# Kernel tuning notes

Hardware: AMD Instinct MI355X
Metric: run time of the kernel (lower is better)

Reference implementation:

```python
import jax, jax.numpy as jnp
import numpy as np

B, T, U, D, NCLS = 4, 256, 128, 512, 1024


def setup_inputs() -> dict:
    key = jax.random.key(0)
    k1, k2, k3, k4, k5, k6 = jax.random.split(key, 6)
    s = 1.0 / np.sqrt(2 * D)  # ~ torch Linear init scale for fan_in=2D
    s2 = 1.0 / np.sqrt(D)
    return {
        "encoder_outputs": jax.random.normal(k1, (B, T, D), jnp.float32),
        "decoder_outputs": jax.random.normal(k2, (B, U, D), jnp.float32),
        "W_e": jax.random.normal(k3, (D, D), jnp.float32) * s,
        "W_d": jax.random.normal(k4, (D, D), jnp.float32) * s,
        "b1": jax.random.normal(k5, (D,), jnp.float32) * s,
        "W2": jax.random.normal(k6, (D, NCLS), jnp.float32) * s2,
    }


def reference(encoder_outputs, decoder_outputs, W_e, W_d, b1, W2):
    # RNNT joint. Original: broadcast-repeat enc to (B,T,U,D) and dec to
    # (B,T,U,D), concat along last dim, Linear(2D->D), tanh, Linear(D->NCLS,
    # no bias), log_softmax. Splitting the first Linear's weight into the
    # encoder half W_e and decoder half W_d gives identical math without
    # materializing the (B,T,U,2D) concat.
    enc_proj = jnp.einsum('btd,dh->bth', encoder_outputs, W_e)  # (B,T,D)
    dec_proj = jnp.einsum('bud,dh->buh', decoder_outputs, W_d)  # (B,U,D)
    hidden = jnp.tanh(enc_proj[:, :, None, :] + dec_proj[:, None, :, :] + b1)  # (B,T,U,D)
    logits = jnp.einsum('btuh,hc->btuc', hidden, W2)  # (B,T,U,NCLS)
    return jax.nn.log_softmax(logits, axis=-1)
```

## Files before the change

### kernel.cpp

```cpp
#include <hip/hip_runtime.h>


#define BB 4
#define TT 256
#define UU 128
#define DD 512
#define CC 1024

using f32x16 = __attribute__((ext_vector_type(16))) float;
using bf16x8 = __attribute__((ext_vector_type(8))) __bf16;

static __device__ __forceinline__ unsigned short f2bf(float f) {
    unsigned int u = __float_as_uint(f);
    unsigned int r = (u + 0x7FFFu + ((u >> 16) & 1u)) >> 16;
    return (unsigned short)r;
}

static __device__ __forceinline__ float tanh_fast(float x) {
    float a = x * 2.8853900817779268f;
    a = fminf(30.f, fmaxf(-30.f, a));
    float e = __expf(a * 0.6931471805599453f);
    float r = __builtin_amdgcn_rcpf(e + 1.0f);
    return __builtin_fmaf(-2.f, r, 1.f);
}

__global__ __launch_bounds__(256) void proj_fused(
    const float* __restrict__ enc, const float* __restrict__ dec,
    const float* __restrict__ W_e, const float* __restrict__ W_d,
    const float* __restrict__ b1,
    float* __restrict__ ep, float* __restrict__ dp)
{
    __shared__ float As[32][34];
    __shared__ float Ws[32][68];
    const int mb = blockIdx.x * 32;
    const int n0 = blockIdx.y * 64;
    const bool is_enc = (mb < BB * TT);
    const float* A = is_enc ? enc + (size_t)mb * DD
                            : dec + (size_t)(mb - BB * TT) * DD;
    const float* W = is_enc ? W_e : W_d;
    float* C = is_enc ? ep + (size_t)mb * DD
                      : dp + (size_t)(mb - BB * TT) * DD;
    const int tid = threadIdx.x;
    const int tx = tid & 15, ty = tid >> 4;
    float acc[2][4] = {};
    for (int k0 = 0; k0 < DD; k0 += 32) {
        __syncthreads();
        {
            const int row = tid >> 3, kk = (tid & 7) * 4;
            float4 v = *reinterpret_cast<const float4*>(A + (size_t)row * DD + k0 + kk);
            As[kk][row] = v.x; As[kk + 1][row] = v.y;
            As[kk + 2][row] = v.z; As[kk + 3][row] = v.w;
            const int wk = tid >> 3, wc2 = (tid & 7) * 8;
            float4 w0 = *reinterpret_cast<const float4*>(W + (size_t)(k0 + wk) * DD + n0 + wc2);
            float4 w1 = *reinterpret_cast<const float4*>(W + (size_t)(k0 + wk) * DD + n0 + wc2 + 4);
            *reinterpret_cast<float4*>(&Ws[wk][wc2]) = w0;
            *reinterpret_cast<float4*>(&Ws[wk][wc2 + 4]) = w1;
        }
        __syncthreads();
        #pragma unroll 4
        for (int kk = 0; kk < 32; ++kk) {
            float a0 = As[kk][ty * 2], a1 = As[kk][ty * 2 + 1];
            float w0 = Ws[kk][tx * 4], w1 = Ws[kk][tx * 4 + 1];
            float w2 = Ws[kk][tx * 4 + 2], w3 = Ws[kk][tx * 4 + 3];
            acc[0][0] += a0 * w0; acc[0][1] += a0 * w1;
            acc[0][2] += a0 * w2; acc[0][3] += a0 * w3;
            acc[1][0] += a1 * w0; acc[1][1] += a1 * w1;
            acc[1][2] += a1 * w2; acc[1][3] += a1 * w3;
        }
    }
    float bb[4] = {0.f, 0.f, 0.f, 0.f};
    if (is_enc) {
        #pragma unroll
        for (int j = 0; j < 4; ++j) bb[j] = b1[n0 + tx * 4 + j];
    }
    #pragma unroll
    for (int i = 0; i < 2; ++i) {
        float4 v;
        v.x = acc[i][0] + bb[0]; v.y = acc[i][1] + bb[1];
        v.z = acc[i][2] + bb[2]; v.w = acc[i][3] + bb[3];
        *reinterpret_cast<float4*>(C + (size_t)(ty * 2 + i) * DD + n0 + tx * 4) = v;
    }
}

__global__ __launch_bounds__(256) void pack_w2(
    const float* __restrict__ W2, unsigned short* __restrict__ w2p)
{
    int i = blockIdx.x * 256 + threadIdx.x;
    int k = i >> 10, c = i & 1023;
    int idx = (((k >> 3) * CC) + c) * 8 + (k & 7);
    w2p[idx] = f2bf(W2[i]);
}

__global__ __launch_bounds__(1024, 4) void joint_kernel(
    const float* __restrict__ ep, const float* __restrict__ dp,
    const unsigned short* __restrict__ w2p, float* __restrict__ out)
{
    __shared__ __align__(16) unsigned char ldsA[64 * 1024];
    __shared__ float maxw[64][9];
    __shared__ float sumw[64][9];

    const int bid = blockIdx.x;
    const int bt  = bid >> 1;
    const int u0  = (bid & 1) * 64;
    const int b   = bt >> 8;
    const int tid = threadIdx.x;

    {
        const int row = tid >> 4;
        const int kq  = tid & 15;
        const float* eprow = ep + (size_t)bt * DD;
        const float* dprow = dp + (size_t)(b * UU + u0 + row) * DD;
        #pragma unroll
        for (int c = 0; c < 4; ++c) {
            const int ktag = kq + c * 16;
            const int k0 = ktag * 8;
            float4 e0 = *reinterpret_cast<const float4*>(eprow + k0);
            float4 e1 = *reinterpret_cast<const float4*>(eprow + k0 + 4);
            float4 d0 = *reinterpret_cast<const float4*>(dprow + k0);
            float4 d1 = *reinterpret_cast<const float4*>(dprow + k0 + 4);
            float h0 = tanh_fast(e0.x + d0.x), h1 = tanh_fast(e0.y + d0.y);
            float h2 = tanh_fast(e0.z + d0.z), h3 = tanh_fast(e0.w + d0.w);
            float h4 = tanh_fast(e1.x + d1.x), h5 = tanh_fast(e1.y + d1.y);
            float h6 = tanh_fast(e1.z + d1.z), h7 = tanh_fast(e1.w + d1.w);
            uint4 pk;
            pk.x = (unsigned)f2bf(h0) | ((unsigned)f2bf(h1) << 16);
            pk.y = (unsigned)f2bf(h2) | ((unsigned)f2bf(h3) << 16);
            pk.z = (unsigned)f2bf(h4) | ((unsigned)f2bf(h5) << 16);
            pk.w = (unsigned)f2bf(h6) | ((unsigned)f2bf(h7) << 16);
            const int rsw = ((row ^ ktag) & 31) | (row & 32);
            *reinterpret_cast<uint4*>(ldsA + ktag * 1024 + rsw * 16) = pk;
        }
    }
    __syncthreads();

    const int lane = tid & 63;
    const int w    = tid >> 6;
    const int g    = lane >> 5;
    const int l31  = lane & 31;
    const int ur   = w >> 3;
    const int wc   = w & 7;

    const unsigned char* hidbase = ldsA + ur * 512;
    const unsigned short* wpbase = w2p + (size_t)(g * 1024 + wc * 128 + l31) * 8;

    f32x16 acc0 = {}, acc1 = {}, acc2 = {}, acc3 = {};

    #define LDH(kk) (*reinterpret_cast<const bf16x8*>(hidbase \
        + ((((kk) & 31) * 2 + g) * 1024) \
        + ((l31 ^ (((((kk) & 31) * 2 + g)) & 31)) << 4)))
    #define LDW(kk, t) (*reinterpret_cast<const bf16x8*>(wpbase \
        + ((size_t)((kk) & 31) * 16384) + (t) * 256))

    bf16x8 wv0 = LDW(0, 0), wv1 = LDW(0, 1), wv2 = LDW(0, 2), wv3 = LDW(0, 3);

    #pragma unroll 2
    for (int kk = 0; kk < 32; ++kk) {
        bf16x8 hf = LDH(kk);
        bf16x8 n0 = LDW(kk + 1, 0), n1 = LDW(kk + 1, 1);
        bf16x8 n2 = LDW(kk + 1, 2), n3 = LDW(kk + 1, 3);
        acc0 = __builtin_amdgcn_mfma_f32_32x32x16_bf16(wv0, hf, acc0, 0, 0, 0);
        acc1 = __builtin_amdgcn_mfma_f32_32x32x16_bf16(wv1, hf, acc1, 0, 0, 0);
        acc2 = __builtin_amdgcn_mfma_f32_32x32x16_bf16(wv2, hf, acc2, 0, 0, 0);
        acc3 = __builtin_amdgcn_mfma_f32_32x32x16_bf16(wv3, hf, acc3, 0, 0, 0);
        wv0 = n0; wv1 = n1; wv2 = n2; wv3 = n3;
    }
    #undef LDH
    #undef LDW

    const int row = ur * 32 + l31;
    float rmloc = -3.0e38f;
    #pragma unroll
    for (int r = 0; r < 16; ++r)
        rmloc = fmaxf(rmloc, fmaxf(fmaxf(acc0[r], acc1[r]), fmaxf(acc2[r], acc3[r])));
    rmloc = fmaxf(rmloc, __shfl_xor(rmloc, 32, 64));
    if (lane < 32) maxw[row][wc] = rmloc;
    __syncthreads();
    float rmax = maxw[row][0];
    #pragma unroll
    for (int j = 1; j < 8; ++j) rmax = fmaxf(rmax, maxw[row][j]);
    float s = 0.f;
    #pragma unroll
    for (int r = 0; r < 16; ++r)
        s += __expf(acc0[r] - rmax) + __expf(acc1[r] - rmax)
           + __expf(acc2[r] - rmax) + __expf(acc3[r] - rmax);
    s += __shfl_xor(s, 32, 64);
    if (lane < 32) sumw[row][wc] = s;
    __syncthreads();
    float tot = 0.f;
    #pragma unroll
    for (int j = 0; j < 8; ++j) tot += sumw[row][j];
    const float lse = rmax + __logf(tot);
    const float lse_r = __shfl(lse, lane >> 1, 64);

    unsigned char* slot = ldsA + w * 4096;
    const int rr = lane >> 1, seg = lane & 1;
    float* outbase = out + ((size_t)(bt * UU + u0 + ur * 32)) * CC + wc * 128;

    #define CHUNK(T, ACC) { \
        _Pragma("unroll") \
        for (int j = 0; j < 4; ++j) { \
            float4 v; \
            v.x = ACC[4 * j]; v.y = ACC[4 * j + 1]; \
            v.z = ACC[4 * j + 2]; v.w = ACC[4 * j + 3]; \
            const int cg = 2 * j + g; \
            *reinterpret_cast<float4*>(slot + l31 * 128 + ((cg ^ (l31 & 7)) << 4)) = v; \
        } \
        asm volatile("s_waitcnt lgkmcnt(0)" ::: "memory"); \
        float4 q0 = *reinterpret_cast<const float4*>(slot + rr * 128 + (((seg * 4 + 0) ^ (rr & 7)) << 4)); \
        float4 q1 = *reinterpret_cast<const float4*>(slot + rr * 128 + (((seg * 4 + 1) ^ (rr & 7)) << 4)); \
        float4 q2 = *reinterpret_cast<const float4*>(slot + rr * 128 + (((seg * 4 + 2) ^ (rr & 7)) << 4)); \
        float4 q3 = *reinterpret_cast<const float4*>(slot + rr * 128 + (((seg * 4 + 3) ^ (rr & 7)) << 4)); \
        float* op = outbase + (size_t)rr * CC + (T) * 32 + seg * 16; \
        q0.x -= lse_r; q0.y -= lse_r; q0.z -= lse_r; q0.w -= lse_r; \
        q1.x -= lse_r; q1.y -= lse_r; q1.z -= lse_r; q1.w -= lse_r; \
        q2.x -= lse_r; q2.y -= lse_r; q2.z -= lse_r; q2.w -= lse_r; \
        q3.x -= lse_r; q3.y -= lse_r; q3.z -= lse_r; q3.w -= lse_r; \
        *reinterpret_cast<float4*>(op + 0)  = q0; \
        *reinterpret_cast<float4*>(op + 4)  = q1; \
        *reinterpret_cast<float4*>(op + 8)  = q2; \
        *reinterpret_cast<float4*>(op + 12) = q3; \
        asm volatile("s_waitcnt lgkmcnt(0)" ::: "memory"); \
    }
    CHUNK(0, acc0)
    CHUNK(1, acc1)
    CHUNK(2, acc2)
    CHUNK(3, acc3)
    #undef CHUNK
}

extern "C" void kernel_launch(void* const* d_in, const int* in_sizes, int n_in,
                              void* d_out, int out_size, void* d_ws, size_t ws_size,
                              hipStream_t stream) {
    const float* enc = (const float*)d_in[0];
    const float* dec = (const float*)d_in[1];
    const float* W_e = (const float*)d_in[2];
    const float* W_d = (const float*)d_in[3];
    const float* b1  = (const float*)d_in[4];
    const float* W2  = (const float*)d_in[5];
    float* out = (float*)d_out;

    char* ws = (char*)d_ws;
    float* ep = (float*)(ws);
    float* dp = (float*)(ws + (2u << 20));
    unsigned short* w2p = (unsigned short*)(ws + (3u << 20));

    hipLaunchKernelGGL(pack_w2, dim3((DD * CC) / 256), dim3(256), 0, stream, W2, w2p);
    hipLaunchKernelGGL(proj_fused, dim3((BB * TT + BB * UU) / 32, DD / 64), dim3(256), 0,
                       stream, enc, dec, W_e, W_d, b1, ep, dp);
    hipLaunchKernelGGL(joint_kernel, dim3(BB * TT * 2), dim3(1024), 0, stream,
                       ep, dp, w2p, out);
}
```

Before: 400.0 us.

## Stage W2 tiles into LDS with double-buffered async loads and retile waves

The joint kernel now streams each 32 KB k-slice of packed W2 into LDS with global_load_lds, double-buffered so the next slice loads during the current MFMAs. Each wave then covers a 64x64 output tile with a 2x2 set of MFMA accumulators, instead of a 32x128 tile fed by per-wave global loads of W2. The intent is to replace redundant per-wave L2 reads of W2 with one shared LDS copy. The output stores also become nontemporal to keep the large log-softmax output from polluting cache. In exchange it adds a block-wide barrier every k step, with only four MFMAs per wave between barriers, and roughly doubles LDS use, which can lower occupancy.

```diff
diff --git a/kernel.cpp b/kernel.cpp
--- a/kernel.cpp
+++ b/kernel.cpp
@@ -8,6 +8,7 @@
 #define CC 1024
 
 using f32x16 = __attribute__((ext_vector_type(16))) float;
+using f32x4  = __attribute__((ext_vector_type(4))) float;
 using bf16x8 = __attribute__((ext_vector_type(8))) __bf16;
 
 static __device__ __forceinline__ unsigned short f2bf(float f) {
@@ -22,6 +23,12 @@
     float e = __expf(a * 0.6931471805599453f);
     float r = __builtin_amdgcn_rcpf(e + 1.0f);
     return __builtin_fmaf(-2.f, r, 1.f);
+}
+
+static __device__ __forceinline__ void gl2lds16(const void* g, void* l) {
+    __builtin_amdgcn_global_load_lds(
+        (const __attribute__((address_space(1))) void*)g,
+        (__attribute__((address_space(3))) void*)l, 16, 0, 0);
 }
 
 __global__ __launch_bounds__(256) void proj_fused(
@@ -91,19 +98,23 @@
     w2p[idx] = f2bf(W2[i]);
 }
 
-__global__ __launch_bounds__(1024, 4) void joint_kernel(
+__global__ __launch_bounds__(1024, 4) void joint_lds(
     const float* __restrict__ ep, const float* __restrict__ dp,
     const unsigned short* __restrict__ w2p, float* __restrict__ out)
 {
-    __shared__ __align__(16) unsigned char ldsA[64 * 1024];
-    __shared__ float maxw[64][9];
-    __shared__ float sumw[64][9];
-
-    const int bid = blockIdx.x;
-    const int bt  = bid >> 1;
-    const int u0  = (bid & 1) * 64;
+    __shared__ __align__(16) unsigned char hidL[64 * 1024];
+    __shared__ __align__(16) unsigned char wbA[32768];
+    __shared__ __align__(16) unsigned char wbB[32768];
+    __shared__ float maxb[64][17];
+    __shared__ float sumb[64][17];
+
+    const int r   = blockIdx.x;
+    const int bt  = r >> 1;
+    const int u0  = (r & 1) * 64;
     const int b   = bt >> 8;
     const int tid = threadIdx.x;
+
+    const unsigned char* w2g = (const unsigned char*)w2p;
 
     {
         const int row = tid >> 4;
@@ -128,8 +139,10 @@
             pk.z = (unsigned)f2bf(h4) | ((unsigned)f2bf(h5) << 16);
             pk.w = (unsigned)f2bf(h6) | ((unsigned)f2bf(h7) << 16);
             const int rsw = ((row ^ ktag) & 31) | (row & 32);
-            *reinterpret_cast<uint4*>(ldsA + ktag * 1024 + rsw * 16) = pk;
-        }
+            *reinterpret_cast<uint4*>(hidL + ktag * 1024 + rsw * 16) = pk;
+        }
+        gl2lds16(w2g + tid * 16,         wbA + tid * 16);
+        gl2lds16(w2g + 16384 + tid * 16, wbA + 16384 + tid * 16);
     }
     __syncthreads();
 
@@ -137,94 +150,97 @@
     const int w    = tid >> 6;
     const int g    = lane >> 5;
     const int l31  = lane & 31;
-    const int ur   = w >> 3;
-    const int wc   = w & 7;
-
-    const unsigned char* hidbase = ldsA + ur * 512;
-    const unsigned short* wpbase = w2p + (size_t)(g * 1024 + wc * 128 + l31) * 8;
-
-    f32x16 acc0 = {}, acc1 = {}, acc2 = {}, acc3 = {};
-
-    #define LDH(kk) (*reinterpret_cast<const bf16x8*>(hidbase \
-        + ((((kk) & 31) * 2 + g) * 1024) \
-        + ((l31 ^ (((((kk) & 31) * 2 + g)) & 31)) << 4)))
-    #define LDW(kk, t) (*reinterpret_cast<const bf16x8*>(wpbase \
-        + ((size_t)((kk) & 31) * 16384) + (t) * 256))
-
-    bf16x8 wv0 = LDW(0, 0), wv1 = LDW(0, 1), wv2 = LDW(0, 2), wv3 = LDW(0, 3);
-
-    #pragma unroll 2
-    for (int kk = 0; kk < 32; ++kk) {
-        bf16x8 hf = LDH(kk);
-        bf16x8 n0 = LDW(kk + 1, 0), n1 = LDW(kk + 1, 1);
-        bf16x8 n2 = LDW(kk + 1, 2), n3 = LDW(kk + 1, 3);
-        acc0 = __builtin_amdgcn_mfma_f32_32x32x16_bf16(wv0, hf, acc0, 0, 0, 0);
-        acc1 = __builtin_amdgcn_mfma_f32_32x32x16_bf16(wv1, hf, acc1, 0, 0, 0);
-        acc2 = __builtin_amdgcn_mfma_f32_32x32x16_bf16(wv2, hf, acc2, 0, 0, 0);
-        acc3 = __builtin_amdgcn_mfma_f32_32x32x16_bf16(wv3, hf, acc3, 0, 0, 0);
-        wv0 = n0; wv1 = n1; wv2 = n2; wv3 = n3;
-    }
-    #undef LDH
-    #undef LDW
-
-    const int row = ur * 32 + l31;
-    float rmloc = -3.0e38f;
-    #pragma unroll
-    for (int r = 0; r < 16; ++r)
-        rmloc = fmaxf(rmloc, fmaxf(fmaxf(acc0[r], acc1[r]), fmaxf(acc2[r], acc3[r])));
-    rmloc = fmaxf(rmloc, __shfl_xor(rmloc, 32, 64));
-    if (lane < 32) maxw[row][wc] = rmloc;
+
+    unsigned char* curb = wbA;
+    unsigned char* nxtb = wbB;
+
+    f32x16 acc00 = {}, acc01 = {}, acc10 = {}, acc11 = {};
+
+    #define MFMA __builtin_amdgcn_mfma_f32_32x32x16_bf16
+    for (int kb = 0; kb < 32; ++kb) {
+        if (kb < 31) {
+            const unsigned char* src = w2g + (size_t)(kb + 1) * 32768;
+            gl2lds16(src + tid * 16,         nxtb + tid * 16);
+            gl2lds16(src + 16384 + tid * 16, nxtb + 16384 + tid * 16);
+        }
+        const int ktag = 2 * kb + g;
+        const int rs = ((l31 ^ ktag) & 31) << 4;
+        bf16x8 h0 = *reinterpret_cast<const bf16x8*>(hidL + ktag * 1024 + rs);
+        bf16x8 h1 = *reinterpret_cast<const bf16x8*>(hidL + ktag * 1024 + 512 + rs);
+        bf16x8 a0 = *reinterpret_cast<const bf16x8*>(curb + ((g * 1024 + w * 64 + l31) << 4));
+        bf16x8 a1 = *reinterpret_cast<const bf16x8*>(curb + ((g * 1024 + w * 64 + 32 + l31) << 4));
+        acc00 = MFMA(a0, h0, acc00, 0, 0, 0);
+        acc01 = MFMA(a0, h1, acc01, 0, 0, 0);
+        acc10 = MFMA(a1, h0, acc10, 0, 0, 0);
+        acc11 = MFMA(a1, h1, acc11, 0, 0, 0);
+        __syncthreads();
+        unsigned char* t = curb; curb = nxtb; nxtb = t;
+    }
+    #undef MFMA
+
+    float m0 = -3.0e38f, m1 = -3.0e38f;
+    #pragma unroll
+    for (int q = 0; q < 16; ++q) {
+        m0 = fmaxf(m0, fmaxf(acc00[q], acc10[q]));
+        m1 = fmaxf(m1, fmaxf(acc01[q], acc11[q]));
+    }
+    m0 = fmaxf(m0, __shfl_xor(m0, 32, 64));
+    m1 = fmaxf(m1, __shfl_xor(m1, 32, 64));
+    if (lane < 32) { maxb[l31][w] = m0; maxb[32 + l31][w] = m1; }
     __syncthreads();
-    float rmax = maxw[row][0];
-    #pragma unroll
-    for (int j = 1; j < 8; ++j) rmax = fmaxf(rmax, maxw[row][j]);
-    float s = 0.f;
-    #pragma unroll
-    for (int r = 0; r < 16; ++r)
-        s += __expf(acc0[r] - rmax) + __expf(acc1[r] - rmax)
-           + __expf(acc2[r] - rmax) + __expf(acc3[r] - rmax);
-    s += __shfl_xor(s, 32, 64);
-    if (lane < 32) sumw[row][wc] = s;
+    float rmax0 = maxb[l31][0], rmax1 = maxb[32 + l31][0];
+    #pragma unroll
+    for (int j = 1; j < 16; ++j) {
+        rmax0 = fmaxf(rmax0, maxb[l31][j]);
+        rmax1 = fmaxf(rmax1, maxb[32 + l31][j]);
+    }
+    float s0 = 0.f, s1 = 0.f;
+    #pragma unroll
+    for (int q = 0; q < 16; ++q) {
+        s0 += __expf(acc00[q] - rmax0) + __expf(acc10[q] - rmax0);
+        s1 += __expf(acc01[q] - rmax1) + __expf(acc11[q] - rmax1);
+    }
+    s0 += __shfl_xor(s0, 32, 64);
+    s1 += __shfl_xor(s1, 32, 64);
+    if (lane < 32) { sumb[l31][w] = s0; sumb[32 + l31][w] = s1; }
     __syncthreads();
-    float tot = 0.f;
-    #pragma unroll
-    for (int j = 0; j < 8; ++j) tot += sumw[row][j];
-    const float lse = rmax + __logf(tot);
-    const float lse_r = __shfl(lse, lane >> 1, 64);
-
-    unsigned char* slot = ldsA + w * 4096;
+    float t0 = 0.f, t1 = 0.f;
+    #pragma unroll
+    for (int j = 0; j < 16; ++j) { t0 += sumb[l31][j]; t1 += sumb[32 + l31][j]; }
+    const float lse0 = rmax0 + __logf(t0);
+    const float lse1 = rmax1 + __logf(t1);
+
+    unsigned char* slot = hidL + w * 4096;
     const int rr = lane >> 1, seg = lane & 1;
-    float* outbase = out + ((size_t)(bt * UU + u0 + ur * 32)) * CC + wc * 128;
-
-    #define CHUNK(T, ACC) { \
+    const float lse_r0 = __shfl(lse0, rr, 64);
+    const float lse_r1 = __shfl(lse1, rr, 64);
+    float* outbase = out + (size_t)r * 64 * CC + w * 64;
+
+    #define CHUNK(MR, T, ACC, LSER) { \
         _Pragma("unroll") \
         for (int j = 0; j < 4; ++j) { \
-            float4 v; \
+            f32x4 v; \
             v.x = ACC[4 * j]; v.y = ACC[4 * j + 1]; \
             v.z = ACC[4 * j + 2]; v.w = ACC[4 * j + 3]; \
-            const int cg = 2 * j + g; \
-            *reinterpret_cast<float4*>(slot + l31 * 128 + ((cg ^ (l31 & 7)) << 4)) = v; \
+            *reinterpret_cast<f32x4*>(slot + l31 * 128 + (((2 * j + g) ^ (l31 & 7)) << 4)) = v; \
         } \
         asm volatile("s_waitcnt lgkmcnt(0)" ::: "memory"); \
-        float4 q0 = *reinterpret_cast<const float4*>(slot + rr * 128 + (((seg * 4 + 0) ^ (rr & 7)) << 4)); \
-        float4 q1 = *reinterpret_cast<const float4*>(slot + rr * 128 + (((seg * 4 + 1) ^ (rr & 7)) << 4)); \
-        float4 q2 = *reinterpret_cast<const float4*>(slot + rr * 128 + (((seg * 4 + 2) ^ (rr & 7)) << 4)); \
-        float4 q3 = *reinterpret_cast<const float4*>(slot + rr * 128 + (((seg * 4 + 3) ^ (rr & 7)) << 4)); \
-        float* op = outbase + (size_t)rr * CC + (T) * 32 + seg * 16; \
-        q0.x -= lse_r; q0.y -= lse_r; q0.z -= lse_r; q0.w -= lse_r; \
-        q1.x -= lse_r; q1.y -= lse_r; q1.z -= lse_r; q1.w -= lse_r; \
-        q2.x -= lse_r; q2.y -= lse_r; q2.z -= lse_r; q2.w -= lse_r; \
-        q3.x -= lse_r; q3.y -= lse_r; q3.z -= lse_r; q3.w -= lse_r; \
-        *reinterpret_cast<float4*>(op + 0)  = q0; \
-        *reinterpret_cast<float4*>(op + 4)  = q1; \
-        *reinterpret_cast<float4*>(op + 8)  = q2; \
-        *reinterpret_cast<float4*>(op + 12) = q3; \
+        f32x4 q0 = *reinterpret_cast<const f32x4*>(slot + rr * 128 + (((seg * 4 + 0) ^ (rr & 7)) << 4)); \
+        f32x4 q1 = *reinterpret_cast<const f32x4*>(slot + rr * 128 + (((seg * 4 + 1) ^ (rr & 7)) << 4)); \
+        f32x4 q2 = *reinterpret_cast<const f32x4*>(slot + rr * 128 + (((seg * 4 + 2) ^ (rr & 7)) << 4)); \
+        f32x4 q3 = *reinterpret_cast<const f32x4*>(slot + rr * 128 + (((seg * 4 + 3) ^ (rr & 7)) << 4)); \
+        float* op = outbase + (size_t)((MR) * 32 + rr) * CC + (T) * 32 + seg * 16; \
+        q0 -= LSER; q1 -= LSER; q2 -= LSER; q3 -= LSER; \
+        __builtin_nontemporal_store(q0, reinterpret_cast<f32x4*>(op + 0)); \
+        __builtin_nontemporal_store(q1, reinterpret_cast<f32x4*>(op + 4)); \
+        __builtin_nontemporal_store(q2, reinterpret_cast<f32x4*>(op + 8)); \
+        __builtin_nontemporal_store(q3, reinterpret_cast<f32x4*>(op + 12)); \
         asm volatile("s_waitcnt lgkmcnt(0)" ::: "memory"); \
     }
-    CHUNK(0, acc0)
-    CHUNK(1, acc1)
-    CHUNK(2, acc2)
-    CHUNK(3, acc3)
+    CHUNK(0, 0, acc00, lse_r0)
+    CHUNK(0, 1, acc10, lse_r0)
+    CHUNK(1, 0, acc01, lse_r1)
+    CHUNK(1, 1, acc11, lse_r1)
     #undef CHUNK
 }
 
@@ -247,6 +263,6 @@
     hipLaunchKernelGGL(pack_w2, dim3((DD * CC) / 256), dim3(256), 0, stream, W2, w2p);
     hipLaunchKernelGGL(proj_fused, dim3((BB * TT + BB * UU) / 32, DD / 64), dim3(256), 0,
                        stream, enc, dec, W_e, W_d, b1, ep, dp);
-    hipLaunchKernelGGL(joint_kernel, dim3(BB * TT * 2), dim3(1024), 0, stream,
+    hipLaunchKernelGGL(joint_lds, dim3(BB * TT * UU / 64), dim3(1024), 0, stream,
                        ep, dp, w2p, out);
 }
```

Measured after the change: 632.4 us. 1.58x slower.
